# Performance work log

Measured on AMD Instinct MI355X. Metric: run time of the kernel, lower is better.

The kernel has to match this reference:

```python
import jax, jax.numpy as jnp
import numpy as np

H = 32        # query heads
KVH = 8       # kv heads
HD = 64       # head_dim
N_REP = H // KVH
THETA = 10000.0


def _rope_cos_sin(seq_len, dim):
    # freqs_cis[t, i] = exp(1j * t * theta^{-2i/dim}) -> return cos, sin [S, dim//2]
    inv_freq = 1.0 / (THETA ** (jnp.arange(0, dim, 2, dtype=jnp.float32) / dim))
    t = jnp.arange(seq_len, dtype=jnp.float32)
    freqs = jnp.outer(t, inv_freq)  # [S, dim//2]
    return jnp.cos(freqs), jnp.sin(freqs)


def _apply_rope(x, cos, sin):
    # x: [B, S, h, HD]; pairs are interleaved (even=real, odd=imag)
    xr = x[..., 0::2]
    xi = x[..., 1::2]
    c = cos[None, :, None, :]
    s = sin[None, :, None, :]
    out_r = xr * c - xi * s
    out_i = xr * s + xi * c
    return jnp.stack([out_r, out_i], axis=-1).reshape(x.shape)


def setup_inputs() -> dict:
    key = jax.random.key(0)
    ks = jax.random.split(key, 5)
    D = 2048
    B, S = 1, 2048
    scale = 0.02
    return {
        "hidden_states": jax.random.normal(ks[0], (B, S, D), jnp.float32),
        "Wq": jax.random.normal(ks[1], (D, H * HD), jnp.float32) * scale,
        "Wk": jax.random.normal(ks[2], (D, KVH * HD), jnp.float32) * scale,
        "Wv": jax.random.normal(ks[3], (D, KVH * HD), jnp.float32) * scale,
        "Wo": jax.random.normal(ks[4], (H * HD, D), jnp.float32) * scale,
    }


def reference(hidden_states, Wq, Wk, Wv, Wo):
    B, S, D = hidden_states.shape
    xq = (hidden_states @ Wq).reshape(B, S, H, HD)
    xk = (hidden_states @ Wk).reshape(B, S, KVH, HD)
    xv = (hidden_states @ Wv).reshape(B, S, KVH, HD)

    cos, sin = _rope_cos_sin(S, HD)
    xq = _apply_rope(xq, cos, sin)
    xk = _apply_rope(xk, cos, sin)

    # GQA: expand kv heads (kv head g -> query heads g*N_REP .. g*N_REP+N_REP-1)
    keys = jnp.repeat(xk, N_REP, axis=2)    # [B, S, H, HD]
    values = jnp.repeat(xv, N_REP, axis=2)

    q = xq.transpose(0, 2, 1, 3)      # [B, H, S, HD]
    k = keys.transpose(0, 2, 1, 3)
    v = values.transpose(0, 2, 1, 3)

    scores = jnp.einsum('bhqd,bhkd->bhqk', q, k) / jnp.sqrt(jnp.float32(HD))
    causal = jnp.tril(jnp.ones((S, S), dtype=bool))
    scores = jnp.where(causal[None, None], scores, jnp.float32(-jnp.inf))
    probs = jax.nn.softmax(scores.astype(jnp.float32), axis=-1).astype(q.dtype)

    out = jnp.einsum('bhqk,bhkd->bhqd', probs, v)   # [B, H, S, HD]
    out = out.transpose(0, 2, 1, 3).reshape(B, S, H * HD)
    return out @ Wo
```

## Files before the change

### kernel.cpp

```cpp
#include <hip/hip_runtime.h>


#define NH  32
#define NKV 8

typedef __attribute__((ext_vector_type(8))) __bf16 bf16x8;
typedef __attribute__((ext_vector_type(4))) __bf16 bf16x4;
typedef __attribute__((ext_vector_type(4))) float  f32x4;

#define SCALE_LOG2 0.18033688011112042f
#define L2_10K_32  0.41524101186098665f

__device__ __forceinline__ void glds16(const __bf16* g, __bf16* l) {
  __builtin_amdgcn_global_load_lds(
      (const __attribute__((address_space(1))) unsigned int*)g,
      (__attribute__((address_space(3))) unsigned int*)l, 16, 0, 0);
}

__device__ __forceinline__ float pair_swap(float v) {
  int t = __builtin_amdgcn_mov_dpp(__builtin_bit_cast(int, v), 0xB1, 0xf, 0xf, true);
  return __builtin_bit_cast(float, t);
}

__device__ __forceinline__ unsigned pack_bf16(float lo, float hi) {
  union { __bf16 b[2]; unsigned u; } r;
  r.b[0] = (__bf16)lo; r.b[1] = (__bf16)hi;
  return r.u;
}

__global__ __launch_bounds__(256) void k_prep(
    const float* __restrict__ hx, const float* __restrict__ Wq,
    const float* __restrict__ Wk, const float* __restrict__ Wv,
    const float* __restrict__ Wo, __bf16* __restrict__ Xb,
    __bf16* __restrict__ Wqkvt, __bf16* __restrict__ Wot) {
  __shared__ float t[32 * 36];
  const int nt = blockIdx.x, k0 = blockIdx.y * 32;
  const int tid = threadIdx.x;
  const int r = tid >> 3, c4 = (tid & 7) * 4;
  if (nt >= 160) {
    int c0 = (nt - 160) * 32;
    float4 v = *(const float4*)(hx + (size_t)(k0 + r) * 2048 + c0 + c4);
    bf16x4 o;
    o[0] = (__bf16)v.x; o[1] = (__bf16)v.y; o[2] = (__bf16)v.z; o[3] = (__bf16)v.w;
    *(bf16x4*)(Xb + (size_t)(k0 + r) * 2048 + c0 + c4) = o;
    return;
  }
  const float* W; int ldW, n0; __bf16* dst;
  if (nt < 64)      { W = Wq; ldW = 2048; dst = Wqkvt;                       n0 = nt * 32; }
  else if (nt < 80) { W = Wk; ldW = 512;  dst = Wqkvt + (size_t)2048 * 2048; n0 = (nt - 64) * 32; }
  else if (nt < 96) { W = Wv; ldW = 512;  dst = Wqkvt + (size_t)2560 * 2048; n0 = (nt - 80) * 32; }
  else              { W = Wo; ldW = 2048; dst = Wot;                         n0 = (nt - 96) * 32; }
  float4 v = *(const float4*)(W + (size_t)(k0 + r) * ldW + n0 + c4);
  *(float4*)(t + r * 36 + ((((c4 >> 2) ^ r) & 7) << 2)) = v;
  __syncthreads();
  bf16x4 o;
#pragma unroll
  for (int j = 0; j < 4; j++) {
    int kk = c4 + j;
    o[j] = (__bf16)t[kk * 36 + ((((r >> 2) ^ kk) & 7) << 2) + (r & 3)];
  }
  *(bf16x4*)(dst + (size_t)(n0 + r) * 2048 + k0 + c4) = o;
}

__global__ void k_vtrans_b(const __bf16* __restrict__ V, __bf16* __restrict__ Vt) {
  __shared__ __bf16 t[32][33];
  int c0 = blockIdx.x * 32, s0 = blockIdx.y * 32;
  int tx = threadIdx.x, ty = threadIdx.y;
#pragma unroll
  for (int j = 0; j < 4; j++)
    t[ty + j * 8][tx] = V[(size_t)(s0 + ty + j * 8) * 512 + c0 + tx];
  __syncthreads();
#pragma unroll
  for (int j = 0; j < 4; j++)
    Vt[(size_t)(c0 + ty + j * 8) * 2048 + s0 + tx] = t[tx][ty + j * 8];
}

__global__ __launch_bounds__(256) void k_gemm_qkv(
    const __bf16* __restrict__ A, const __bf16* __restrict__ Bt,
    __bf16* __restrict__ Qb, __bf16* __restrict__ Kb, __bf16* __restrict__ Vb) {
  const int K = 2048;
  __shared__ __bf16 As[64][64];
  __shared__ __bf16 Bs[128][64];
  const int tid = threadIdx.x;
  const int m0 = blockIdx.x * 64, n0 = blockIdx.y * 128;
  const int w = tid >> 6, lane = tid & 63, quad = lane >> 4, lid = lane & 15;
  const int wm = (w & 1) * 32, wn = (w >> 1) * 64;
  const int r0 = tid >> 3;
  const int cg0 = (((tid & 7) ^ (r0 & 7)) * 8);
  const __bf16* Ag = A + (size_t)(m0 + r0) * K + cg0;
  const __bf16* Bg = Bt + (size_t)(n0 + r0) * K + cg0;
  __bf16* Asl = &As[0][0] + tid * 8;
  __bf16* Bsl = &Bs[0][0] + tid * 8;
  const int cl = ((quad ^ (lid & 7)) * 8);
  f32x4 acc[2][4] = {};
  for (int k0 = 0; k0 < K; k0 += 64) {
    __syncthreads();
    glds16(Ag + k0, Asl);
    glds16(Ag + (size_t)32 * K + k0, Asl + 2048);
    glds16(Bg + k0, Bsl);
    glds16(Bg + (size_t)32 * K + k0, Bsl + 2048);
    glds16(Bg + (size_t)64 * K + k0, Bsl + 4096);
    glds16(Bg + (size_t)96 * K + k0, Bsl + 6144);
    __syncthreads();
    bf16x8 a[2][2], b[4][2];
#pragma unroll
    for (int mt = 0; mt < 2; mt++) {
      a[mt][0] = *(const bf16x8*)(&As[wm + mt * 16 + lid][cl]);
      a[mt][1] = *(const bf16x8*)(&As[wm + mt * 16 + lid][cl ^ 32]);
    }
#pragma unroll
    for (int nt = 0; nt < 4; nt++) {
      b[nt][0] = *(const bf16x8*)(&Bs[wn + nt * 16 + lid][cl]);
      b[nt][1] = *(const bf16x8*)(&Bs[wn + nt * 16 + lid][cl ^ 32]);
    }
#pragma unroll
    for (int mt = 0; mt < 2; mt++)
#pragma unroll
      for (int nt = 0; nt < 4; nt++) {
        acc[mt][nt] = __builtin_amdgcn_mfma_f32_16x16x32_bf16(
            a[mt][0], b[nt][0], acc[mt][nt], 0, 0, 0);
        acc[mt][nt] = __builtin_amdgcn_mfma_f32_16x16x32_bf16(
            a[mt][1], b[nt][1], acc[mt][nt], 0, 0, 0);
      }
  }
  if (n0 >= 2560) {
#pragma unroll
    for (int mt = 0; mt < 2; mt++)
#pragma unroll
      for (int nt = 0; nt < 4; nt++)
#pragma unroll
        for (int i = 0; i < 4; i++) {
          int mm = m0 + wm + mt * 16 + quad * 4 + i;
          int nn = n0 + wn + nt * 16 + lid - 2560;
          Vb[(size_t)mm * 512 + nn] = (__bf16)acc[mt][nt][i];
        }
  } else {
    const bool isQ = (n0 < 2048);
    const float scale = isQ ? SCALE_LOG2 : 1.0f;
    __bf16* dst = isQ ? Qb : Kb;
    const int ldd = isQ ? 2048 : 512;
    const int noff = isQ ? 0 : 2048;
    const bool odd = lid & 1;
#pragma unroll
    for (int nt = 0; nt < 4; nt++) {
      int nn = n0 + wn + nt * 16 + lid;
      int fi = (nn & 63) >> 1;
      float inv = __builtin_amdgcn_exp2f(-(float)fi * L2_10K_32);
#pragma unroll
      for (int mt = 0; mt < 2; mt++)
#pragma unroll
        for (int i = 0; i < 4; i++) {
          int mm = m0 + wm + mt * 16 + quad * 4 + i;
          float ang = (float)mm * inv;
          float sn, cs;
          __sincosf(ang, &sn, &cs);
          float v = acc[mt][nt][i];
          float p = __shfl_xor(v, 1);
          float o = v * cs + (odd ? p : -p) * sn;
          dst[(size_t)mm * ldd + nn - noff] = (__bf16)(o * scale);
        }
    }
  }
}

__global__ __launch_bounds__(256) void k_gemm_out(
    const __bf16* __restrict__ A, const __bf16* __restrict__ Bt,
    float* __restrict__ C) {
  const int K = 2048, N = 2048;
  __shared__ __bf16 As[64][64];
  __shared__ __bf16 Bs[128][64];
  const int tid = threadIdx.x;
  const int m0 = blockIdx.x * 64, n0 = blockIdx.y * 128;
  const int w = tid >> 6, lane = tid & 63, quad = lane >> 4, lid = lane & 15;
  const int wm = (w & 1) * 32, wn = (w >> 1) * 64;
  const int r0 = tid >> 3;
  const int cg0 = (((tid & 7) ^ (r0 & 7)) * 8);
  const __bf16* Ag = A + (size_t)(m0 + r0) * K + cg0;
  const __bf16* Bg = Bt + (size_t)(n0 + r0) * K + cg0;
  __bf16* Asl = &As[0][0] + tid * 8;
  __bf16* Bsl = &Bs[0][0] + tid * 8;
  const int cl = ((quad ^ (lid & 7)) * 8);
  f32x4 acc[2][4] = {};
  for (int k0 = 0; k0 < K; k0 += 64) {
    __syncthreads();
    glds16(Ag + k0, Asl);
    glds16(Ag + (size_t)32 * K + k0, Asl + 2048);
    glds16(Bg + k0, Bsl);
    glds16(Bg + (size_t)32 * K + k0, Bsl + 2048);
    glds16(Bg + (size_t)64 * K + k0, Bsl + 4096);
    glds16(Bg + (size_t)96 * K + k0, Bsl + 6144);
    __syncthreads();
    bf16x8 a[2][2], b[4][2];
#pragma unroll
    for (int mt = 0; mt < 2; mt++) {
      a[mt][0] = *(const bf16x8*)(&As[wm + mt * 16 + lid][cl]);
      a[mt][1] = *(const bf16x8*)(&As[wm + mt * 16 + lid][cl ^ 32]);
    }
#pragma unroll
    for (int nt = 0; nt < 4; nt++) {
      b[nt][0] = *(const bf16x8*)(&Bs[wn + nt * 16 + lid][cl]);
      b[nt][1] = *(const bf16x8*)(&Bs[wn + nt * 16 + lid][cl ^ 32]);
    }
#pragma unroll
    for (int mt = 0; mt < 2; mt++)
#pragma unroll
      for (int nt = 0; nt < 4; nt++) {
        acc[mt][nt] = __builtin_amdgcn_mfma_f32_16x16x32_bf16(
            a[mt][0], b[nt][0], acc[mt][nt], 0, 0, 0);
        acc[mt][nt] = __builtin_amdgcn_mfma_f32_16x16x32_bf16(
            a[mt][1], b[nt][1], acc[mt][nt], 0, 0, 0);
      }
  }
#pragma unroll
  for (int mt = 0; mt < 2; mt++)
#pragma unroll
    for (int nt = 0; nt < 4; nt++)
#pragma unroll
      for (int i = 0; i < 4; i++) {
        int mm = m0 + wm + mt * 16 + quad * 4 + i;
        int nn = n0 + wn + nt * 16 + lid;
        C[(size_t)mm * N + nn] = acc[mt][nt][i];
      }
}

__global__ __launch_bounds__(256, 4) void k_attn(
    const __bf16* __restrict__ Q, const __bf16* __restrict__ Kc,
    const __bf16* __restrict__ Vt, __bf16* __restrict__ Oc) {
  __shared__ __bf16 Ps[4][32][40];
  __shared__ float OL[2][32][68];
  __shared__ float Lsh[64];
  const int h = blockIdx.x;
  const int qt = 31 - blockIdx.y;
  const int q0 = qt * 64;
  const int kvh = h >> 2;
  const int tid = threadIdx.x;
  const int w = tid >> 6, lane = tid & 63, quad = lane >> 4, lid = lane & 15;
  const int qh = w & 1, kh = w >> 1;

  bf16x8 aq[2][2];
#pragma unroll
  for (int mt = 0; mt < 2; mt++)
#pragma unroll
    for (int ks = 0; ks < 2; ks++)
      aq[mt][ks] = *(const bf16x8*)(
          Q + (size_t)(q0 + qh * 32 + mt * 16 + lid) * 2048 + h * 64 +
          ks * 32 + quad * 8);

  bf16x8 bone;
#pragma unroll
  for (int j = 0; j < 8; j++) bone[j] = (lid == 0) ? (__bf16)1.0f : (__bf16)0.0f;

  const __bf16* Kfr = Kc + (size_t)(kh * 32 + lid) * 512 + kvh * 64 + quad * 8;
  const __bf16* Vfr = Vt + (size_t)(kvh * 64 + lid) * 2048 + kh * 32 + quad * 8;

  f32x4 Oacc[2][4] = {};
  f32x4 Lacc[2] = {};

  for (int kt = 0; kt <= qt; kt++) {
    const int kv0 = kt * 64;
    bf16x8 kf[2][2];
#pragma unroll
    for (int nt = 0; nt < 2; nt++)
#pragma unroll
      for (int ch = 0; ch < 2; ch++)
        kf[nt][ch] = *(const bf16x8*)(Kfr + (size_t)(kv0 + nt * 16) * 512 + ch * 32);
    bf16x8 vf[4];
#pragma unroll
    for (int nt = 0; nt < 4; nt++)
      vf[nt] = *(const bf16x8*)(Vfr + (size_t)nt * 16 * 2048 + kv0);

    f32x4 Sc[2][2] = {};
#pragma unroll
    for (int nt = 0; nt < 2; nt++)
#pragma unroll
      for (int mt = 0; mt < 2; mt++) {
        Sc[mt][nt] = __builtin_amdgcn_mfma_f32_16x16x32_bf16(
            aq[mt][0], kf[nt][0], Sc[mt][nt], 0, 0, 0);
        Sc[mt][nt] = __builtin_amdgcn_mfma_f32_16x16x32_bf16(
            aq[mt][1], kf[nt][1], Sc[mt][nt], 0, 0, 0);
      }
    if (kt == qt) {
#pragma unroll
      for (int mt = 0; mt < 2; mt++)
#pragma unroll
        for (int nt = 0; nt < 2; nt++)
#pragma unroll
          for (int i = 0; i < 4; i++) {
            int kvg = kv0 + kh * 32 + nt * 16 + lid;
            int qrg = q0 + qh * 32 + mt * 16 + quad * 4 + i;
            if (kvg > qrg) Sc[mt][nt][i] = -1e30f;
          }
    }

#pragma unroll
    for (int mt = 0; mt < 2; mt++)
#pragma unroll
      for (int i = 0; i < 4; i++) {
        float pA = __builtin_amdgcn_exp2f(Sc[mt][0][i]);
        float pB = __builtin_amdgcn_exp2f(Sc[mt][1][i]);
        float send = (lid & 1) ? pA : pB;
        float recv = pair_swap(send);
        float lo = (lid & 1) ? recv : pA;
        float hi = (lid & 1) ? pB : recv;
        int row = mt * 16 + quad * 4 + i;
        int col = (lid & 1) ? (lid + 15) : lid;
        *(unsigned*)(&Ps[w][row][col]) = pack_bf16(lo, hi);
      }

    bf16x8 ap[2];
#pragma unroll
    for (int mt = 0; mt < 2; mt++)
      ap[mt] = *(const bf16x8*)(&Ps[w][mt * 16 + lid][quad * 8]);
#pragma unroll
    for (int mt = 0; mt < 2; mt++)
      Lacc[mt] = __builtin_amdgcn_mfma_f32_16x16x32_bf16(ap[mt], bone, Lacc[mt], 0, 0, 0);
#pragma unroll
    for (int nt = 0; nt < 4; nt++)
#pragma unroll
      for (int mt = 0; mt < 2; mt++)
        Oacc[mt][nt] = __builtin_amdgcn_mfma_f32_16x16x32_bf16(
            ap[mt], vf[nt], Oacc[mt][nt], 0, 0, 0);
  }

  if (kh == 1) {
#pragma unroll
    for (int mt = 0; mt < 2; mt++)
#pragma unroll
      for (int nt = 0; nt < 4; nt++)
#pragma unroll
        for (int i = 0; i < 4; i++)
          OL[qh][mt * 16 + quad * 4 + i][nt * 16 + lid] = Oacc[mt][nt][i];
    if (lid == 0)
#pragma unroll
      for (int mt = 0; mt < 2; mt++)
#pragma unroll
        for (int i = 0; i < 4; i++)
          Lsh[qh * 32 + mt * 16 + quad * 4 + i] = Lacc[mt][i];
  }
  __syncthreads();
  if (kh == 0) {
#pragma unroll
    for (int mt = 0; mt < 2; mt++)
#pragma unroll
      for (int i = 0; i < 4; i++) {
        int row = mt * 16 + quad * 4 + i;
        float lsum = __shfl(Lacc[mt][i], lane & 48) + Lsh[qh * 32 + row];
        float rs = 1.0f / lsum;
#pragma unroll
        for (int nt = 0; nt < 4; nt++) {
          float o = Oacc[mt][nt][i] + OL[qh][row][nt * 16 + lid];
          Oc[(size_t)(q0 + qh * 32 + row) * 2048 + h * 64 + nt * 16 + lid] =
              (__bf16)(o * rs);
        }
      }
  }
}

extern "C" void kernel_launch(void* const* d_in, const int* in_sizes, int n_in,
                              void* d_out, int out_size, void* d_ws, size_t ws_size,
                              hipStream_t stream) {
  const float* hx = (const float*)d_in[0];
  const float* Wq = (const float*)d_in[1];
  const float* Wk = (const float*)d_in[2];
  const float* Wv = (const float*)d_in[3];
  const float* Wo = (const float*)d_in[4];
  float* out = (float*)d_out;

  char* ws = (char*)d_ws;
  size_t off = 0;
  auto alloc = [&](size_t bytes) -> void* {
    void* p = ws + off;
    off += (bytes + 255) & ~(size_t)255;
    return p;
  };
  __bf16* Xb    = (__bf16*)alloc((size_t)2048 * 2048 * 2);
  __bf16* Wqkvt = (__bf16*)alloc((size_t)3072 * 2048 * 2);
  __bf16* Wot   = (__bf16*)alloc((size_t)2048 * 2048 * 2);
  __bf16* Qb    = (__bf16*)alloc((size_t)2048 * 2048 * 2);
  __bf16* Kb    = (__bf16*)alloc((size_t)2048 * 512 * 2);
  __bf16* Vb    = (__bf16*)alloc((size_t)2048 * 512 * 2);
  __bf16* Vtg   = (__bf16*)alloc((size_t)512 * 2048 * 2);
  __bf16* AOb   = (__bf16*)alloc((size_t)2048 * 2048 * 2);

  k_prep<<<dim3(224, 64), 256, 0, stream>>>(hx, Wq, Wk, Wv, Wo, Xb, Wqkvt, Wot);
  k_gemm_qkv<<<dim3(32, 24), 256, 0, stream>>>(Xb, Wqkvt, Qb, Kb, Vb);
  k_vtrans_b<<<dim3(16, 64), dim3(32, 8), 0, stream>>>(Vb, Vtg);
  k_attn<<<dim3(NH, 32), 256, 0, stream>>>(Qb, Kb, Vtg, AOb);
  k_gemm_out<<<dim3(32, 16), 256, 0, stream>>>(AOb, Wot, out);
}
```

Before: 239.5 us.

## Stage K/V tiles in double-buffered swizzled LDS via async global-to-LDS loads

The attention kernel now loads each 64-row K and V tile cooperatively into shared memory with global_load_lds, using an XOR-swizzled layout and double buffering so the next tile's load overlaps the current tile's MFMA work. Fragments are then read from LDS instead of straight from global memory, which removes redundant per-wave global loads. The cost is a larger LDS footprint, with occupancy lowered from 4 to 3 blocks per SM, and a block-wide barrier every iteration. The epilogue buffers are aliased onto the same shared memory region.

```diff
diff --git a/kernel.cpp b/kernel.cpp
--- a/kernel.cpp
+++ b/kernel.cpp
@@ -223,12 +223,15 @@
       }
 }
 
-__global__ __launch_bounds__(256, 4) void k_attn(
+__global__ __launch_bounds__(256, 3) void k_attn(
     const __bf16* __restrict__ Q, const __bf16* __restrict__ Kc,
     const __bf16* __restrict__ Vt, __bf16* __restrict__ Oc) {
-  __shared__ __bf16 Ps[4][32][40];
-  __shared__ float OL[2][32][68];
-  __shared__ float Lsh[64];
+  __shared__ char smem[43008];
+  __bf16* KsB = (__bf16*)smem;
+  __bf16* VsB = (__bf16*)(smem + 16384);
+  __bf16* PsB = (__bf16*)(smem + 32768);
+  float*  OL  = (float*)smem;
+  float*  Lsh = (float*)(smem + 17408);
   const int h = blockIdx.x;
   const int qt = 31 - blockIdx.y;
   const int q0 = qt * 64;
@@ -236,6 +239,8 @@
   const int tid = threadIdx.x;
   const int w = tid >> 6, lane = tid & 63, quad = lane >> 4, lid = lane & 15;
   const int qh = w & 1, kh = w >> 1;
+  const int r0 = tid >> 3;
+  const int cg0 = (((tid & 7) ^ (r0 & 7)) * 8);
 
   bf16x8 aq[2][2];
 #pragma unroll
@@ -250,35 +255,43 @@
 #pragma unroll
   for (int j = 0; j < 8; j++) bone[j] = (lid == 0) ? (__bf16)1.0f : (__bf16)0.0f;
 
-  const __bf16* Kfr = Kc + (size_t)(kh * 32 + lid) * 512 + kvh * 64 + quad * 8;
-  const __bf16* Vfr = Vt + (size_t)(kvh * 64 + lid) * 2048 + kh * 32 + quad * 8;
+  const __bf16* Kg = Kc + kvh * 64 + cg0;
+  const __bf16* Vg = Vt + ((size_t)(kvh * 64 + r0)) * 2048 + cg0;
+  __bf16* Pw = PsB + w * 1280;
+
+  glds16(Kg + (size_t)r0 * 512,        KsB + tid * 8);
+  glds16(Kg + (size_t)(r0 + 32) * 512, KsB + (tid + 256) * 8);
+  glds16(Vg,                           VsB + tid * 8);
+  glds16(Vg + (size_t)32 * 2048,       VsB + (tid + 256) * 8);
+  __syncthreads();
 
   f32x4 Oacc[2][4] = {};
   f32x4 Lacc[2] = {};
 
   for (int kt = 0; kt <= qt; kt++) {
-    const int kv0 = kt * 64;
-    bf16x8 kf[2][2];
-#pragma unroll
-    for (int nt = 0; nt < 2; nt++)
-#pragma unroll
-      for (int ch = 0; ch < 2; ch++)
-        kf[nt][ch] = *(const bf16x8*)(Kfr + (size_t)(kv0 + nt * 16) * 512 + ch * 32);
-    bf16x8 vf[4];
-#pragma unroll
-    for (int nt = 0; nt < 4; nt++)
-      vf[nt] = *(const bf16x8*)(Vfr + (size_t)nt * 16 * 2048 + kv0);
+    const int cb = kt & 1;
+    if (kt < qt) {
+      const int nb = cb ^ 1;
+      const size_t kv1 = (size_t)(kt + 1) * 64;
+      glds16(Kg + (kv1 + r0) * 512,        KsB + nb * 4096 + tid * 8);
+      glds16(Kg + (kv1 + r0 + 32) * 512,   KsB + nb * 4096 + (tid + 256) * 8);
+      glds16(Vg + kv1,                     VsB + nb * 4096 + tid * 8);
+      glds16(Vg + (size_t)32 * 2048 + kv1, VsB + nb * 4096 + (tid + 256) * 8);
+    }
 
     f32x4 Sc[2][2] = {};
 #pragma unroll
-    for (int nt = 0; nt < 2; nt++)
+    for (int nt = 0; nt < 2; nt++) {
+      int krow = kh * 32 + nt * 16 + lid;
+      int cl = (quad ^ (lid & 7)) * 8;
+      bf16x8 b0 = *(const bf16x8*)(KsB + cb * 4096 + krow * 64 + cl);
+      bf16x8 b1 = *(const bf16x8*)(KsB + cb * 4096 + krow * 64 + (cl ^ 32));
 #pragma unroll
       for (int mt = 0; mt < 2; mt++) {
-        Sc[mt][nt] = __builtin_amdgcn_mfma_f32_16x16x32_bf16(
-            aq[mt][0], kf[nt][0], Sc[mt][nt], 0, 0, 0);
-        Sc[mt][nt] = __builtin_amdgcn_mfma_f32_16x16x32_bf16(
-            aq[mt][1], kf[nt][1], Sc[mt][nt], 0, 0, 0);
-      }
+        Sc[mt][nt] = __builtin_amdgcn_mfma_f32_16x16x32_bf16(aq[mt][0], b0, Sc[mt][nt], 0, 0, 0);
+        Sc[mt][nt] = __builtin_amdgcn_mfma_f32_16x16x32_bf16(aq[mt][1], b1, Sc[mt][nt], 0, 0, 0);
+      }
+    }
     if (kt == qt) {
 #pragma unroll
       for (int mt = 0; mt < 2; mt++)
@@ -286,7 +299,7 @@
         for (int nt = 0; nt < 2; nt++)
 #pragma unroll
           for (int i = 0; i < 4; i++) {
-            int kvg = kv0 + kh * 32 + nt * 16 + lid;
+            int kvg = kt * 64 + kh * 32 + nt * 16 + lid;
             int qrg = q0 + qh * 32 + mt * 16 + quad * 4 + i;
             if (kvg > qrg) Sc[mt][nt][i] = -1e30f;
           }
@@ -304,22 +317,25 @@
         float hi = (lid & 1) ? pB : recv;
         int row = mt * 16 + quad * 4 + i;
         int col = (lid & 1) ? (lid + 15) : lid;
-        *(unsigned*)(&Ps[w][row][col]) = pack_bf16(lo, hi);
+        *(unsigned*)(Pw + row * 40 + col) = pack_bf16(lo, hi);
       }
 
     bf16x8 ap[2];
 #pragma unroll
     for (int mt = 0; mt < 2; mt++)
-      ap[mt] = *(const bf16x8*)(&Ps[w][mt * 16 + lid][quad * 8]);
+      ap[mt] = *(const bf16x8*)(Pw + (mt * 16 + lid) * 40 + quad * 8);
 #pragma unroll
     for (int mt = 0; mt < 2; mt++)
       Lacc[mt] = __builtin_amdgcn_mfma_f32_16x16x32_bf16(ap[mt], bone, Lacc[mt], 0, 0, 0);
 #pragma unroll
-    for (int nt = 0; nt < 4; nt++)
+    for (int nt = 0; nt < 4; nt++) {
+      bf16x8 bv = *(const bf16x8*)(
+          VsB + cb * 4096 + (nt * 16 + lid) * 64 + (((kh * 4 + quad) ^ (lid & 7)) * 8));
 #pragma unroll
       for (int mt = 0; mt < 2; mt++)
-        Oacc[mt][nt] = __builtin_amdgcn_mfma_f32_16x16x32_bf16(
-            ap[mt], vf[nt], Oacc[mt][nt], 0, 0, 0);
+        Oacc[mt][nt] = __builtin_amdgcn_mfma_f32_16x16x32_bf16(ap[mt], bv, Oacc[mt][nt], 0, 0, 0);
+    }
+    __syncthreads();
   }
 
   if (kh == 1) {
@@ -329,7 +345,8 @@
       for (int nt = 0; nt < 4; nt++)
 #pragma unroll
         for (int i = 0; i < 4; i++)
-          OL[qh][mt * 16 + quad * 4 + i][nt * 16 + lid] = Oacc[mt][nt][i];
+          OL[qh * 2176 + (mt * 16 + quad * 4 + i) * 68 + nt * 16 + lid] =
+              Oacc[mt][nt][i];
     if (lid == 0)
 #pragma unroll
       for (int mt = 0; mt < 2; mt++)
@@ -348,7 +365,7 @@
         float rs = 1.0f / lsum;
 #pragma unroll
         for (int nt = 0; nt < 4; nt++) {
-          float o = Oacc[mt][nt][i] + OL[qh][row][nt * 16 + lid];
+          float o = Oacc[mt][nt][i] + OL[qh * 2176 + row * 68 + nt * 16 + lid];
           Oc[(size_t)(q0 + qh * 32 + row) * 2048 + h * 64 + nt * 16 + lid] =
               (__bf16)(o * rs);
         }
```

New measurement: 198.3 us. 17.2% less time.
